# Performance work log

Hardware: AMD Instinct MI355X
Metric: run time of the kernel (lower is better)

## Reference

```python
import jax, jax.numpy as jnp
import numpy as np

IMG = 8       # image_size
LH = 150      # l_h
LQ = 10       # l_q
K = 10        # value-iteration steps
B = 16384     # batch
N_STATES = 2 + IMG * IMG


def _conv(x, w, pad):
    # NCHW conv, stride 1
    return jax.lax.conv_general_dilated(
        x, w, window_strides=(1, 1), padding=[(pad, pad), (pad, pad)],
        dimension_numbers=('NCHW', 'OIHW', 'NCHW'))


def setup_inputs() -> dict:
    key = jax.random.key(0)
    ks = jax.random.split(key, 8)
    grid = jax.random.normal(ks[0], (B, IMG * IMG), dtype=jnp.float32)
    pos = jax.random.randint(ks[1], (B, 2), 0, IMG).astype(jnp.float32)
    S = jnp.concatenate([grid, pos], axis=1)                      # [B, 66]
    Wh = jax.random.normal(ks[2], (LH, 1, 3, 3), jnp.float32) * 0.1
    bh = jnp.zeros((LH,), jnp.float32)
    Wr = jax.random.normal(ks[3], (1, LH, 1, 1), jnp.float32) * 0.1
    Wq = jax.random.normal(ks[4], (LQ, 1, 3, 3), jnp.float32) * 0.1
    w = jax.random.normal(ks[5], (LQ, 1, 3, 3), jnp.float32) * 0.1
    Wfc = jax.random.normal(ks[6], (8, LQ), jnp.float32) * 0.1
    return {'S': S, 'Wh': Wh, 'bh': bh, 'Wr': Wr, 'Wq': Wq, 'w': w, 'Wfc': Wfc}


def reference(S, Wh, bh, Wr, Wq, w, Wfc):
    X = S[:, :IMG * IMG].reshape(-1, 1, IMG, IMG)                 # [B,1,8,8]
    s1 = S[:, IMG * IMG].astype(jnp.int32)                        # row index
    s2 = S[:, IMG * IMG + 1].astype(jnp.int32)                    # col index

    h = _conv(X, Wh, 1) + bh[None, :, None, None]                 # [B,150,8,8]
    r = _conv(h, Wr, 0)                                           # [B,1,8,8]
    q = _conv(r, Wq, 1)                                           # [B,10,8,8]
    v = jnp.max(q, axis=1, keepdims=True)                         # [B,1,8,8]

    Wcat = jnp.concatenate([Wq, w], axis=1)                       # [10,2,3,3]

    def step(v, _):
        qq = _conv(jnp.concatenate([r, v], axis=1), Wcat, 1)
        return jnp.max(qq, axis=1, keepdims=True), None

    v, _ = jax.lax.scan(step, v, None, length=K - 1)
    q = _conv(jnp.concatenate([r, v], axis=1), Wcat, 1)           # [B,10,8,8]

    bidx = jnp.arange(q.shape[0])
    q_sel = q[bidx, :, s1, s2]                                    # [B,10]
    logits = q_sel @ Wfc.T                                        # [B,8]
    return logits
```

## Files before the change

kernel.cpp:

```cpp
#include <hip/hip_runtime.h>

#define IMG 8
#define LH 150
#define LQ 10
#define KITER 10
#define ROW (IMG * IMG + 2)

typedef float f32x2 __attribute__((ext_vector_type(2)));

__device__ __forceinline__ float bperm(int byte_addr, float v) {
    return __builtin_bit_cast(float,
        __builtin_amdgcn_ds_bpermute(byte_addr, __builtin_bit_cast(int, v)));
}

template <int CTRL>
__device__ __forceinline__ float dppf(float v) {
    return __builtin_bit_cast(float,
        __builtin_amdgcn_update_dpp(0, __builtin_bit_cast(int, v),
                                    CTRL, 0xF, 0xF, true));
}
#define DPP_SHR1 0x111
#define DPP_SHL1 0x101

__device__ __forceinline__ f32x2 fma2(f32x2 a, f32x2 b, f32x2 c) {
#if __has_builtin(__builtin_elementwise_fma)
    return __builtin_elementwise_fma(a, b, c);
#else
    return a * b + c;
#endif
}
__device__ __forceinline__ f32x2 max2(f32x2 a, f32x2 b) {
    f32x2 r; r.x = fmaxf(a.x, b.x); r.y = fmaxf(a.y, b.y); return r;
}

__device__ __forceinline__ void gather9(f32x2 vn[9], f32x2 v, int aU, int aD) {
    f32x2 vU, vD;
    vU.x = bperm(aU, v.x); vU.y = bperm(aU, v.y);
    vD.x = bperm(aD, v.x); vD.y = bperm(aD, v.y);
    vn[1] = vU; vn[4] = v; vn[7] = vD;
    vn[0].x = dppf<DPP_SHR1>(vU.x); vn[0].y = dppf<DPP_SHR1>(vU.y);
    vn[2].x = dppf<DPP_SHL1>(vU.x); vn[2].y = dppf<DPP_SHL1>(vU.y);
    vn[3].x = dppf<DPP_SHR1>(v.x);  vn[3].y = dppf<DPP_SHR1>(v.y);
    vn[5].x = dppf<DPP_SHL1>(v.x);  vn[5].y = dppf<DPP_SHL1>(v.y);
    vn[6].x = dppf<DPP_SHR1>(vD.x); vn[6].y = dppf<DPP_SHR1>(vD.y);
    vn[8].x = dppf<DPP_SHL1>(vD.x); vn[8].y = dppf<DPP_SHL1>(vD.y);
}

__global__ void weff_kernel(const float* __restrict__ Wh,
                            const float* __restrict__ bh,
                            const float* __restrict__ Wr,
                            float* __restrict__ ws) {
    const int wv = threadIdx.x >> 6;
    const int lane = threadIdx.x & 63;
    float partial = 0.f;
    for (int c = lane; c < LH; c += 64) {
        const float wr = Wr[c];
        partial += wr * ((wv < 9) ? Wh[c * 9 + wv] : bh[c]);
    }
    #pragma unroll
    for (int off = 32; off > 0; off >>= 1)
        partial += __shfl_xor(partial, off);
    if (lane == 0) ws[wv] = partial;
}

__global__ __launch_bounds__(256, 2) void vin_kernel(
    const float* __restrict__ S,
    const float* __restrict__ Wq,
    const float* __restrict__ w,
    const float* __restrict__ Wfc,
    const float* __restrict__ ws,
    float* __restrict__ out,
    int B) {
    const int wave = threadIdx.x >> 6;
    const int lane = threadIdx.x & 63;
    const long b0 = (long)(blockIdx.x * 4 + wave) * 2;
    if (b0 >= B) return;

    const int y = lane >> 3, x = lane & 7;

    float msk[9];
    #pragma unroll
    for (int t = 0; t < 9; ++t) {
        const int ny = y + t / 3 - 1, nx = x + t % 3 - 1;
        msk[t] = (((unsigned)ny < 8u) && ((unsigned)nx < 8u)) ? 1.f : 0.f;
    }
    const int aU = ((y > 0) ? (lane - 8) : 0) << 2;
    const int aD = ((y < 7) ? (lane + 8) : 0) << 2;

    const float* S0 = S + b0 * ROW;
    f32x2 X; X.x = S0[lane]; X.y = S0[ROW + lane];
    const int sel0 = ((int)S0[IMG * IMG] * 8 + (int)S0[IMG * IMG + 1]) << 2;
    const int sel1 = ((int)S0[ROW + IMG * IMG] * 8 + (int)S0[ROW + IMG * IMG + 1]) << 2;

    f32x2 r;
    {
        f32x2 xn[9]; gather9(xn, X, aU, aD);
        const float b = ws[9];
        r.x = b; r.y = b;
        #pragma unroll
        for (int t = 0; t < 9; ++t) {
            const float wm = ws[t] * msk[t];
            f32x2 w2; w2.x = wm; w2.y = wm;
            r = fma2(xn[t], w2, r);
        }
    }

    f32x2 qr[LQ];
    {
        f32x2 rn[9]; gather9(rn, r, aU, aD);
        #pragma unroll
        for (int t = 0; t < 9; ++t) {
            f32x2 a; a.x = rn[t].x * msk[t]; a.y = rn[t].y * msk[t];
            #pragma unroll
            for (int o = 0; o < LQ; ++o) {
                const float wq = Wq[o * 9 + t];
                f32x2 w2; w2.x = wq; w2.y = wq;
                qr[o] = (t == 0) ? (a * w2) : fma2(a, w2, qr[o]);
            }
        }
    }

    f32x2 wp[LQ][9];
    #pragma unroll
    for (int o = 0; o < LQ; ++o)
        #pragma unroll
        for (int t = 0; t < 9; ++t) {
            const float wm = w[o * 9 + t] * msk[t];
            wp[o][t].x = wm; wp[o][t].y = wm;
        }

    f32x2 v;
    {
        const f32x2 g0 = max2(max2(qr[0], qr[1]), qr[2]);
        const f32x2 g1 = max2(max2(qr[3], qr[4]), qr[5]);
        const f32x2 g2 = max2(max2(qr[6], qr[7]), qr[8]);
        v = max2(max2(g0, g1), max2(g2, qr[9]));
    }

    #pragma unroll
    for (int k = 0; k < KITER - 1; ++k) {
        f32x2 vn[9]; gather9(vn, v, aU, aD);
        f32x2 m;
        #pragma unroll
        for (int o = 0; o < LQ; ++o) {
            f32x2 acc = qr[o];
            #pragma unroll
            for (int t = 0; t < 9; ++t)
                acc = fma2(vn[t], wp[o][t], acc);
            m = (o == 0) ? acc : max2(m, acc);
        }
        v = m;
    }

    float oacc = 0.f;
    {
        f32x2 vn[9]; gather9(vn, v, aU, aD);
        const int row = lane & 7;
        #pragma unroll
        for (int o = 0; o < LQ; ++o) {
            f32x2 acc = qr[o];
            #pragma unroll
            for (int t = 0; t < 9; ++t)
                acc = fma2(vn[t], wp[o][t], acc);
            const float q0 = bperm(sel0, acc.x);
            const float q1 = bperm(sel1, acc.y);
            oacc = fmaf((lane < 8) ? q0 : q1, Wfc[row * LQ + o], oacc);
        }
    }
    if (lane < 16) out[b0 * 8 + lane] = oacc;
}

extern "C" void kernel_launch(void* const* d_in, const int* in_sizes, int n_in,
                              void* d_out, int out_size, void* d_ws, size_t ws_size,
                              hipStream_t stream) {
    const float* S   = (const float*)d_in[0];
    const float* Wh  = (const float*)d_in[1];
    const float* bh  = (const float*)d_in[2];
    const float* Wr  = (const float*)d_in[3];
    const float* Wq  = (const float*)d_in[4];
    const float* w   = (const float*)d_in[5];
    const float* Wfc = (const float*)d_in[6];
    float* out = (float*)d_out;
    float* ws  = (float*)d_ws;

    const int B = in_sizes[0] / ROW;

    weff_kernel<<<1, 640, 0, stream>>>(Wh, bh, Wr, ws);

    const int grid = (B + 7) / 8;
    vin_kernel<<<grid, 256, 0, stream>>>(S, Wq, w, Wfc, ws, out, B);
}
```

Measured before the change: 91.83 us.

## Keep uniform recurrence weights in scalar registers and apply boundary mask to neighbors

The recurrence weights are no longer stored as per-lane masked f32x2 vector registers (180 VGPRs). They are made wave-uniform via readfirstlane so the compiler can hold them in SGPRs. The boundary mask is instead applied to the 8 gathered neighbor values once per iteration, which adds a few multiplies. This frees vector registers, and the launch bound is raised to 6 blocks per CU to increase occupancy; the risk is SGPR pressure or spills and extra VALU work per iteration.

Result: slower. 101.3 us (+10.3%).

```diff
diff --git a/kernel.cpp b/kernel.cpp
--- a/kernel.cpp
+++ b/kernel.cpp
@@ -11,6 +11,11 @@
 __device__ __forceinline__ float bperm(int byte_addr, float v) {
     return __builtin_bit_cast(float,
         __builtin_amdgcn_ds_bpermute(byte_addr, __builtin_bit_cast(int, v)));
+}
+
+__device__ __forceinline__ float rfl(float v) {
+    return __builtin_bit_cast(float,
+        __builtin_amdgcn_readfirstlane(__builtin_bit_cast(int, v)));
 }
 
 template <int CTRL>
@@ -30,7 +35,15 @@
 #endif
 }
 __device__ __forceinline__ f32x2 max2(f32x2 a, f32x2 b) {
+#if __has_builtin(__builtin_elementwise_max)
+    return __builtin_elementwise_max(a, b);
+#else
     f32x2 r; r.x = fmaxf(a.x, b.x); r.y = fmaxf(a.y, b.y); return r;
+#endif
+}
+__device__ __forceinline__ f32x2 set2(float s) { f32x2 r; r.x = s; r.y = s; return r; }
+__device__ __forceinline__ f32x2 mulm(f32x2 v, float m) {
+    f32x2 r; r.x = v.x * m; r.y = v.y * m; return r;
 }
 
 __device__ __forceinline__ void gather9(f32x2 vn[9], f32x2 v, int aU, int aD) {
@@ -63,7 +76,7 @@
     if (lane == 0) ws[wv] = partial;
 }
 
-__global__ __launch_bounds__(256, 2) void vin_kernel(
+__global__ __launch_bounds__(256, 6) void vin_kernel(
     const float* __restrict__ S,
     const float* __restrict__ Wq,
     const float* __restrict__ w,
@@ -96,12 +109,11 @@
     {
         f32x2 xn[9]; gather9(xn, X, aU, aD);
         const float b = ws[9];
-        r.x = b; r.y = b;
+        r = set2(b);
         #pragma unroll
         for (int t = 0; t < 9; ++t) {
             const float wm = ws[t] * msk[t];
-            f32x2 w2; w2.x = wm; w2.y = wm;
-            r = fma2(xn[t], w2, r);
+            r = fma2(xn[t], set2(wm), r);
         }
     }
 
@@ -110,24 +122,21 @@
         f32x2 rn[9]; gather9(rn, r, aU, aD);
         #pragma unroll
         for (int t = 0; t < 9; ++t) {
-            f32x2 a; a.x = rn[t].x * msk[t]; a.y = rn[t].y * msk[t];
+            const f32x2 a = mulm(rn[t], msk[t]);
             #pragma unroll
             for (int o = 0; o < LQ; ++o) {
                 const float wq = Wq[o * 9 + t];
-                f32x2 w2; w2.x = wq; w2.y = wq;
-                qr[o] = (t == 0) ? (a * w2) : fma2(a, w2, qr[o]);
+                qr[o] = (t == 0) ? (a * set2(wq)) : fma2(a, set2(wq), qr[o]);
             }
         }
     }
 
-    f32x2 wp[LQ][9];
+    float wu[LQ][9];
     #pragma unroll
     for (int o = 0; o < LQ; ++o)
         #pragma unroll
-        for (int t = 0; t < 9; ++t) {
-            const float wm = w[o * 9 + t] * msk[t];
-            wp[o][t].x = wm; wp[o][t].y = wm;
-        }
+        for (int t = 0; t < 9; ++t)
+            wu[o][t] = rfl(w[o * 9 + t]);
 
     f32x2 v;
     {
@@ -140,13 +149,16 @@
     #pragma unroll
     for (int k = 0; k < KITER - 1; ++k) {
         f32x2 vn[9]; gather9(vn, v, aU, aD);
+        #pragma unroll
+        for (int t = 0; t < 9; ++t)
+            if (t != 4) vn[t] = mulm(vn[t], msk[t]);
         f32x2 m;
         #pragma unroll
         for (int o = 0; o < LQ; ++o) {
             f32x2 acc = qr[o];
             #pragma unroll
             for (int t = 0; t < 9; ++t)
-                acc = fma2(vn[t], wp[o][t], acc);
+                acc = fma2(vn[t], set2(wu[o][t]), acc);
             m = (o == 0) ? acc : max2(m, acc);
         }
         v = m;
@@ -155,13 +167,16 @@
     float oacc = 0.f;
     {
         f32x2 vn[9]; gather9(vn, v, aU, aD);
+        #pragma unroll
+        for (int t = 0; t < 9; ++t)
+            if (t != 4) vn[t] = mulm(vn[t], msk[t]);
         const int row = lane & 7;
         #pragma unroll
         for (int o = 0; o < LQ; ++o) {
             f32x2 acc = qr[o];
             #pragma unroll
             for (int t = 0; t < 9; ++t)
-                acc = fma2(vn[t], wp[o][t], acc);
+                acc = fma2(vn[t], set2(wu[o][t]), acc);
             const float q0 = bperm(sel0, acc.x);
             const float q1 = bperm(sel1, acc.y);
             oacc = fmaf((lane < 8) ? q0 : q1, Wfc[row * LQ + o], oacc);
```

## Remap lanes to 4 images per wave with 4-row strips per lane

Applied to the files above, without the earlier changes.

Each wave now processes 4 batch images, with 16 lanes per image and each lane owning a 4-row column strip. Vertical neighbours now come from in-register rows plus row_shr/shl:8 DPP, replacing ds_bpermute gathers, and horizontal taps use DPP shifts with edge masks. The per-lane weight registers (wp) are dropped in favour of scalar weight reads, occupancy bounds go from 2 to 4 blocks per CU, and the value-iteration loop is no longer unrolled. Final selection uses a one-hot row blend followed by a single bpermute. The aim is to cut cross-lane traffic and register pressure, at the cost of more scalar weight loads and less ILP from dropping the f32x2 packing and loop unroll.

After: 99.43 us. 1.08x slower.

```diff
diff --git a/kernel.cpp b/kernel.cpp
--- a/kernel.cpp
+++ b/kernel.cpp
@@ -6,8 +6,6 @@
 #define KITER 10
 #define ROW (IMG * IMG + 2)
 
-typedef float f32x2 __attribute__((ext_vector_type(2)));
-
 __device__ __forceinline__ float bperm(int byte_addr, float v) {
     return __builtin_bit_cast(float,
         __builtin_amdgcn_ds_bpermute(byte_addr, __builtin_bit_cast(int, v)));
@@ -21,29 +19,20 @@
 }
 #define DPP_SHR1 0x111
 #define DPP_SHL1 0x101
-
-__device__ __forceinline__ f32x2 fma2(f32x2 a, f32x2 b, f32x2 c) {
-#if __has_builtin(__builtin_elementwise_fma)
-    return __builtin_elementwise_fma(a, b, c);
-#else
-    return a * b + c;
-#endif
-}
-__device__ __forceinline__ f32x2 max2(f32x2 a, f32x2 b) {
-    f32x2 r; r.x = fmaxf(a.x, b.x); r.y = fmaxf(a.y, b.y); return r;
-}
-
-__device__ __forceinline__ void gather9(f32x2 vn[9], f32x2 v, int aU, int aD) {
-    f32x2 vU, vD;
-    vU.x = bperm(aU, v.x); vU.y = bperm(aU, v.y);
-    vD.x = bperm(aD, v.x); vD.y = bperm(aD, v.y);
-    vn[1] = vU; vn[4] = v; vn[7] = vD;
-    vn[0].x = dppf<DPP_SHR1>(vU.x); vn[0].y = dppf<DPP_SHR1>(vU.y);
-    vn[2].x = dppf<DPP_SHL1>(vU.x); vn[2].y = dppf<DPP_SHL1>(vU.y);
-    vn[3].x = dppf<DPP_SHR1>(v.x);  vn[3].y = dppf<DPP_SHR1>(v.y);
-    vn[5].x = dppf<DPP_SHL1>(v.x);  vn[5].y = dppf<DPP_SHL1>(v.y);
-    vn[6].x = dppf<DPP_SHR1>(vD.x); vn[6].y = dppf<DPP_SHR1>(vD.y);
-    vn[8].x = dppf<DPP_SHL1>(vD.x); vn[8].y = dppf<DPP_SHL1>(vD.y);
+#define DPP_SHR8 0x118
+#define DPP_SHL8 0x108
+
+__device__ __forceinline__ void taps6(const float v[4], float C[6],
+                                      float L[6], float R6[6],
+                                      float mskL, float mskR) {
+    C[0] = dppf<DPP_SHR8>(v[3]);
+    C[1] = v[0]; C[2] = v[1]; C[3] = v[2]; C[4] = v[3];
+    C[5] = dppf<DPP_SHL8>(v[0]);
+    #pragma unroll
+    for (int j = 0; j < 6; ++j) {
+        L[j]  = mskL * dppf<DPP_SHR1>(C[j]);
+        R6[j] = mskR * dppf<DPP_SHL1>(C[j]);
+    }
 }
 
 __global__ void weff_kernel(const float* __restrict__ Wh,
@@ -63,7 +52,7 @@
     if (lane == 0) ws[wv] = partial;
 }
 
-__global__ __launch_bounds__(256, 2) void vin_kernel(
+__global__ __launch_bounds__(256, 4) void vin_kernel(
     const float* __restrict__ S,
     const float* __restrict__ Wq,
     const float* __restrict__ w,
@@ -73,101 +62,144 @@
     int B) {
     const int wave = threadIdx.x >> 6;
     const int lane = threadIdx.x & 63;
-    const long b0 = (long)(blockIdx.x * 4 + wave) * 2;
+    const long b0 = (long)(blockIdx.x * 4 + wave) * 4;
     if (b0 >= B) return;
 
-    const int y = lane >> 3, x = lane & 7;
-
-    float msk[9];
-    #pragma unroll
-    for (int t = 0; t < 9; ++t) {
-        const int ny = y + t / 3 - 1, nx = x + t % 3 - 1;
-        msk[t] = (((unsigned)ny < 8u) && ((unsigned)nx < 8u)) ? 1.f : 0.f;
-    }
-    const int aU = ((y > 0) ? (lane - 8) : 0) << 2;
-    const int aD = ((y < 7) ? (lane + 8) : 0) << 2;
-
-    const float* S0 = S + b0 * ROW;
-    f32x2 X; X.x = S0[lane]; X.y = S0[ROW + lane];
-    const int sel0 = ((int)S0[IMG * IMG] * 8 + (int)S0[IMG * IMG + 1]) << 2;
-    const int sel1 = ((int)S0[ROW + IMG * IMG] * 8 + (int)S0[ROW + IMG * IMG + 1]) << 2;
-
-    f32x2 r;
+    const int grp  = lane >> 4;
+    const int half = (lane >> 3) & 1;
+    const int x    = lane & 7;
+    const float mskL = (x > 0) ? 1.f : 0.f;
+    const float mskR = (x < 7) ? 1.f : 0.f;
+
+    const long b = b0 + grp;
+    const float* Sb = S + b * ROW;
+
+    float v[4];
+    #pragma unroll
+    for (int yr = 0; yr < 4; ++yr)
+        v[yr] = Sb[(half * 4 + yr) * 8 + x];
+    const int s1i = (int)Sb[IMG * IMG];
+    const int s2i = (int)Sb[IMG * IMG + 1];
+    const int selAddr = ((grp << 4) + ((s1i & 4) << 1) + s2i) << 2;
+
     {
-        f32x2 xn[9]; gather9(xn, X, aU, aD);
-        const float b = ws[9];
-        r.x = b; r.y = b;
-        #pragma unroll
-        for (int t = 0; t < 9; ++t) {
-            const float wm = ws[t] * msk[t];
-            f32x2 w2; w2.x = wm; w2.y = wm;
-            r = fma2(xn[t], w2, r);
-        }
-    }
-
-    f32x2 qr[LQ];
+        float C[6], L[6], R6[6];
+        taps6(v, C, L, R6, mskL, mskR);
+        const float bias = ws[9];
+        #pragma unroll
+        for (int yr = 0; yr < 4; ++yr) {
+            float a = bias;
+            #pragma unroll
+            for (int ky = 0; ky < 3; ++ky) {
+                const int j = yr + ky;
+                a = fmaf(L[j],  ws[ky * 3 + 0], a);
+                a = fmaf(C[j],  ws[ky * 3 + 1], a);
+                a = fmaf(R6[j], ws[ky * 3 + 2], a);
+            }
+            v[yr] = a;
+        }
+    }
+
+    float qr[LQ][4];
     {
-        f32x2 rn[9]; gather9(rn, r, aU, aD);
-        #pragma unroll
-        for (int t = 0; t < 9; ++t) {
-            f32x2 a; a.x = rn[t].x * msk[t]; a.y = rn[t].y * msk[t];
+        float C[6], L[6], R6[6];
+        taps6(v, C, L, R6, mskL, mskR);
+        #pragma unroll
+        for (int o = 0; o < LQ; ++o) {
             #pragma unroll
-            for (int o = 0; o < LQ; ++o) {
-                const float wq = Wq[o * 9 + t];
-                f32x2 w2; w2.x = wq; w2.y = wq;
-                qr[o] = (t == 0) ? (a * w2) : fma2(a, w2, qr[o]);
-            }
-        }
-    }
-
-    f32x2 wp[LQ][9];
-    #pragma unroll
-    for (int o = 0; o < LQ; ++o)
-        #pragma unroll
-        for (int t = 0; t < 9; ++t) {
-            const float wm = w[o * 9 + t] * msk[t];
-            wp[o][t].x = wm; wp[o][t].y = wm;
-        }
-
-    f32x2 v;
+            for (int yr = 0; yr < 4; ++yr) {
+                float a = L[yr] * Wq[o * 9 + 0];
+                a = fmaf(C[yr],      Wq[o * 9 + 1], a);
+                a = fmaf(R6[yr],     Wq[o * 9 + 2], a);
+                a = fmaf(L[yr + 1],  Wq[o * 9 + 3], a);
+                a = fmaf(C[yr + 1],  Wq[o * 9 + 4], a);
+                a = fmaf(R6[yr + 1], Wq[o * 9 + 5], a);
+                a = fmaf(L[yr + 2],  Wq[o * 9 + 6], a);
+                a = fmaf(C[yr + 2],  Wq[o * 9 + 7], a);
+                a = fmaf(R6[yr + 2], Wq[o * 9 + 8], a);
+                qr[o][yr] = a;
+            }
+        }
+    }
+
+    #pragma unroll
+    for (int yr = 0; yr < 4; ++yr) {
+        const float g0 = fmaxf(fmaxf(qr[0][yr], qr[1][yr]), qr[2][yr]);
+        const float g1 = fmaxf(fmaxf(qr[3][yr], qr[4][yr]), qr[5][yr]);
+        const float g2 = fmaxf(fmaxf(qr[6][yr], qr[7][yr]), qr[8][yr]);
+        v[yr] = fmaxf(fmaxf(g0, g1), fmaxf(g2, qr[9][yr]));
+    }
+
+    #pragma unroll 1
+    for (int k = 0; k < KITER - 1; ++k) {
+        float C[6], L[6], R6[6];
+        taps6(v, C, L, R6, mskL, mskR);
+        float q[LQ][4];
+        #pragma unroll
+        for (int o = 0; o < LQ; ++o) {
+            #pragma unroll
+            for (int yr = 0; yr < 4; ++yr) {
+                float a = qr[o][yr];
+                a = fmaf(L[yr],      w[o * 9 + 0], a);
+                a = fmaf(C[yr],      w[o * 9 + 1], a);
+                a = fmaf(R6[yr],     w[o * 9 + 2], a);
+                a = fmaf(L[yr + 1],  w[o * 9 + 3], a);
+                a = fmaf(C[yr + 1],  w[o * 9 + 4], a);
+                a = fmaf(R6[yr + 1], w[o * 9 + 5], a);
+                a = fmaf(L[yr + 2],  w[o * 9 + 6], a);
+                a = fmaf(C[yr + 2],  w[o * 9 + 7], a);
+                a = fmaf(R6[yr + 2], w[o * 9 + 8], a);
+                q[o][yr] = a;
+            }
+        }
+        #pragma unroll
+        for (int yr = 0; yr < 4; ++yr) {
+            const float g0 = fmaxf(fmaxf(q[0][yr], q[1][yr]), q[2][yr]);
+            const float g1 = fmaxf(fmaxf(q[3][yr], q[4][yr]), q[5][yr]);
+            const float g2 = fmaxf(fmaxf(q[6][yr], q[7][yr]), q[8][yr]);
+            v[yr] = fmaxf(fmaxf(g0, g1), fmaxf(g2, q[9][yr]));
+        }
+    }
+
+    float e[4];
+    #pragma unroll
+    for (int yr = 0; yr < 4; ++yr)
+        e[yr] = (s1i == half * 4 + yr) ? 1.f : 0.f;
+
+    const int row = lane & 7;
+    float osum = 0.f;
     {
-        const f32x2 g0 = max2(max2(qr[0], qr[1]), qr[2]);
-        const f32x2 g1 = max2(max2(qr[3], qr[4]), qr[5]);
-        const f32x2 g2 = max2(max2(qr[6], qr[7]), qr[8]);
-        v = max2(max2(g0, g1), max2(g2, qr[9]));
-    }
-
-    #pragma unroll
-    for (int k = 0; k < KITER - 1; ++k) {
-        f32x2 vn[9]; gather9(vn, v, aU, aD);
-        f32x2 m;
+        float C[6], L[6], R6[6];
+        taps6(v, C, L, R6, mskL, mskR);
         #pragma unroll
         for (int o = 0; o < LQ; ++o) {
-            f32x2 acc = qr[o];
-            #pragma unroll
-            for (int t = 0; t < 9; ++t)
-                acc = fma2(vn[t], wp[o][t], acc);
-            m = (o == 0) ? acc : max2(m, acc);
-        }
-        v = m;
-    }
-
-    float oacc = 0.f;
-    {
-        f32x2 vn[9]; gather9(vn, v, aU, aD);
-        const int row = lane & 7;
-        #pragma unroll
-        for (int o = 0; o < LQ; ++o) {
-            f32x2 acc = qr[o];
-            #pragma unroll
-            for (int t = 0; t < 9; ++t)
-                acc = fma2(vn[t], wp[o][t], acc);
-            const float q0 = bperm(sel0, acc.x);
-            const float q1 = bperm(sel1, acc.y);
-            oacc = fmaf((lane < 8) ? q0 : q1, Wfc[row * LQ + o], oacc);
-        }
-    }
-    if (lane < 16) out[b0 * 8 + lane] = oacc;
+            float t;
+            {
+                float ayr[4];
+                #pragma unroll
+                for (int yr = 0; yr < 4; ++yr) {
+                    float a = qr[o][yr];
+                    a = fmaf(L[yr],      w[o * 9 + 0], a);
+                    a = fmaf(C[yr],      w[o * 9 + 1], a);
+                    a = fmaf(R6[yr],     w[o * 9 + 2], a);
+                    a = fmaf(L[yr + 1],  w[o * 9 + 3], a);
+                    a = fmaf(C[yr + 1],  w[o * 9 + 4], a);
+                    a = fmaf(R6[yr + 1], w[o * 9 + 5], a);
+                    a = fmaf(L[yr + 2],  w[o * 9 + 6], a);
+                    a = fmaf(C[yr + 2],  w[o * 9 + 7], a);
+                    a = fmaf(R6[yr + 2], w[o * 9 + 8], a);
+                    ayr[yr] = a;
+                }
+                t = ayr[0] * e[0];
+                t = fmaf(ayr[1], e[1], t);
+                t = fmaf(ayr[2], e[2], t);
+                t = fmaf(ayr[3], e[3], t);
+            }
+            const float qs = bperm(selAddr, t);
+            osum = fmaf(qs, Wfc[row * LQ + o], osum);
+        }
+    }
+    if ((lane & 15) < 8) out[b * 8 + row] = osum;
 }
 
 extern "C" void kernel_launch(void* const* d_in, const int* in_sizes, int n_in,
@@ -187,6 +219,6 @@
 
     weff_kernel<<<1, 640, 0, stream>>>(Wh, bh, Wr, ws);
 
-    const int grid = (B + 7) / 8;
+    const int grid = (B + 15) / 16;
     vin_kernel<<<grid, 256, 0, stream>>>(S, Wq, w, Wfc, ws, out, B);
 }
```
